# Optimization experiments

Measured on AMD Instinct MI355X. Metric: run time of the kernel, lower is better.

Reference implementation:

```python
import jax, jax.numpy as jnp
import numpy as np

# ---- static config (matches init_kwargs) ----
D = 1152      # hidden_size
I = 4608      # mlp intermediate = 4*D
DEPTH = 2     # transformer blocks
SA_DEPTH = 3  # spatial adapter depth
P_LAT = 2     # latent patch size
OUT_C = 8     # in_channels*2 (learn_sigma)
FREQ = 256    # timestep frequency embedding size
NV = 4        # num_views
B = 2         # true batch (BN = B*NV = 8)
LAT = 32      # latent H=W
COND = 512    # conditioning image H=W

# ---- BitNet b1.58 / HGRN primitives ----

def rmsnorm(x, eps=1e-8):
    return x * jax.lax.rsqrt(jnp.mean(jnp.square(x), axis=-1, keepdims=True) + eps)

def layernorm(x, gamma=None, beta=None, eps=1e-6):
    mu = jnp.mean(x, axis=-1, keepdims=True)
    xc = x - mu
    y = xc * jax.lax.rsqrt(jnp.mean(jnp.square(xc), axis=-1, keepdims=True) + eps)
    if gamma is not None:
        y = y * gamma + beta
    return y

def _act_quant(x):  # per-token int8 absmax quantization
    s = 127.0 / jnp.clip(jnp.max(jnp.abs(x), axis=-1, keepdims=True), 1e-5, None)
    return jnp.clip(jnp.round(x * s), -128.0, 127.0) / s

def _w_quant(w):    # ternary (1.58-bit) weight quantization, global absmean scale
    s = 1.0 / jnp.clip(jnp.mean(jnp.abs(w)), 1e-5, None)
    return jnp.clip(jnp.round(w * s), -1.0, 1.0) / s

def _ste(x, q):     # straight-through estimator
    return x + jax.lax.stop_gradient(q - x)

def bitlinear(x, w, b=None):
    # FusedBitLinear: RMSNorm -> int8 act quant -> ternary weight matmul
    xn = rmsnorm(x)
    y = _ste(xn, _act_quant(xn)) @ _ste(w, _w_quant(w)).T
    return y if b is None else y + b

def conv2d(x, w, b, stride):
    y = jax.lax.conv_general_dilated(x, w, (stride, stride), 'VALID',
                                     dimension_numbers=('NCHW', 'OIHW', 'NCHW'))
    return y + b[None, :, None, None]

def hgrn_attn(x, wi, wf, wg, wo):
    # HGRN gated-linear attention: h_t = f_t*h_{t-1} + silu(i_t)*(1-f_t),
    # output RMSNorm-swish-gated then o-projected. Element-wise recurrence.
    f = jax.nn.sigmoid(bitlinear(x, wf))
    v = jax.nn.silu(bitlinear(x, wi)) * (1.0 - f)
    g = bitlinear(x, wg)
    def step(h, fv):
        ft, vt = fv
        h = ft * h + vt
        return h, h
    _, o = jax.lax.scan(step, jnp.zeros_like(v[:, 0]),
                        (jnp.swapaxes(f, 0, 1), jnp.swapaxes(v, 0, 1)))
    o = jnp.swapaxes(o, 0, 1)
    o = rmsnorm(o) * g * jax.nn.sigmoid(g)
    return bitlinear(o, wo)

def hgrn_mlp(x, w_gate, w_down):
    gate, y = jnp.split(bitlinear(x, w_gate), 2, axis=-1)
    return bitlinear(jax.nn.silu(gate) * y, w_down)

def modulate(x, shift, scale):
    return x * (1.0 + scale[:, None]) + shift[:, None]

# ---- full adapter forward ----

def _forward(x, t, y, x_cond, ref_tokens, num_views, P):
    BN = x.shape[0]
    # conditioning vector c = TimestepEmbedder(t) + prompt_proj(y)
    half = FREQ // 2
    freqs = jnp.exp(-np.log(10000.0) * jnp.arange(half, dtype=jnp.float32) / half)
    ang = t[:, None] * freqs[None]
    t_emb = jnp.concatenate([jnp.cos(ang), jnp.sin(ang)], axis=-1)
    t_emb = bitlinear(jax.nn.silu(bitlinear(t_emb, P['te_w1'], P['te_b1'])), P['te_w2'], P['te_b2'])
    c = t_emb + bitlinear(y, P['pp_w'], P['pp_b'])

    h = conv2d(x_cond, P['sa_pe_w'], P['sa_pe_b'], 16)      # [BN, D, 32, 32]
    Hc = h.shape[-1]
    h = h.reshape(BN, D, Hc * Hc).transpose(0, 2, 1)
    feats = []
    for i in range(SA_DEPTH):
        h = hgrn_mlp(layernorm(h, P['sa_ln_g'][i], P['sa_ln_b'][i], eps=1e-5),
                     P['sa_gate_w'][i], P['sa_down_w'][i])
        h = h.transpose(0, 2, 1).reshape(BN, D, Hc, Hc)
        h = conv2d(h, P['sa_dc_w'][i], P['sa_dc_b'][i], 2)
        Hc //= 2
        h = h.reshape(BN, D, Hc * Hc).transpose(0, 2, 1)
        feats.append(h)

    # patchify latents + pos embed + spatial cond feature (grid-matched)
    xt = conv2d(x, P['xe_w'], P['xe_b'], P_LAT)             # [BN, D, 16, 16]
    Hp = xt.shape[-1]
    xt = xt.reshape(BN, D, Hp * Hp).transpose(0, 2, 1) + P['pos_embed'] + feats[0]
    L = xt.shape[1]
    b = BN // num_views
    ref_rep = jnp.repeat(ref_tokens, num_views, axis=0)     # repeat_interleave dim 0

    for l in range(DEPTH):
        mod = bitlinear(jax.nn.silu(c), P['blk_ada_w'][l], P['blk_ada_b'][l])
        sh_a, sc_a, g_a, sh_m, sc_m, g_m = jnp.split(mod, 6, axis=-1)
        xm = modulate(layernorm(xt), sh_a, sc_a)
        self_out = hgrn_attn(xm, P['blk_sa_wi'][l], P['blk_sa_wf'][l], P['blk_sa_wg'][l], P['blk_sa_wo'][l])
        # multi-view attention: sequence axis = views
        mv_in = xm.reshape(b, num_views, L, D).transpose(0, 2, 1, 3).reshape(b * L, num_views, D)
        mv_out = hgrn_attn(mv_in, P['blk_mv_wi'][l], P['blk_mv_wf'][l], P['blk_mv_wg'][l], P['blk_mv_wo'][l])
        mv_out = mv_out.reshape(b, L, num_views, D).transpose(0, 2, 1, 3).reshape(BN, L, D)
        ref_out = hgrn_attn(ref_rep, P['blk_rf_wi'][l], P['blk_rf_wf'][l], P['blk_rf_wg'][l], P['blk_rf_wo'][l])
        xt = xt + g_a[:, None] * (self_out + mv_out + ref_out)
        xm = modulate(layernorm(xt), sh_m, sc_m)
        xt = xt + g_m[:, None] * hgrn_mlp(xm, P['blk_gate_w'][l], P['blk_down_w'][l])

    # final layer + unpatchify
    mod = bitlinear(jax.nn.silu(c), P['fl_ada_w'], P['fl_ada_b'])
    shift, scale = jnp.split(mod, 2, axis=-1)
    xt = bitlinear(modulate(layernorm(xt), shift, scale), P['fl_w'], P['fl_b'])
    xt = xt.reshape(BN, Hp, Hp, P_LAT, P_LAT, OUT_C).transpose(0, 5, 1, 3, 2, 4)
    return xt.reshape(BN, OUT_C, Hp * P_LAT, Hp * P_LAT)

PARAM_SHAPES = {
    'xe_w': (D, 4, P_LAT, P_LAT), 'xe_b': (D,), 'pos_embed': (1, 256, D),
    'te_w1': (D, FREQ), 'te_b1': (D,), 'te_w2': (D, D), 'te_b2': (D,),
    'pp_w': (D, 768), 'pp_b': (D,),
    'sa_pe_w': (D, 6, 16, 16), 'sa_pe_b': (D,),
    'sa_ln_g': (SA_DEPTH, D), 'sa_ln_b': (SA_DEPTH, D),
    'sa_gate_w': (SA_DEPTH, 2 * I, D), 'sa_down_w': (SA_DEPTH, D, I),
    'sa_dc_w': (SA_DEPTH, D, D, 2, 2), 'sa_dc_b': (SA_DEPTH, D),
    'blk_ada_w': (DEPTH, 6 * D, D), 'blk_ada_b': (DEPTH, 6 * D),
    'blk_sa_wi': (DEPTH, D, D), 'blk_sa_wf': (DEPTH, D, D), 'blk_sa_wg': (DEPTH, D, D), 'blk_sa_wo': (DEPTH, D, D),
    'blk_mv_wi': (DEPTH, D, D), 'blk_mv_wf': (DEPTH, D, D), 'blk_mv_wg': (DEPTH, D, D), 'blk_mv_wo': (DEPTH, D, D),
    'blk_rf_wi': (DEPTH, D, D), 'blk_rf_wf': (DEPTH, D, D), 'blk_rf_wg': (DEPTH, D, D), 'blk_rf_wo': (DEPTH, D, D),
    'blk_gate_w': (DEPTH, 2 * I, D), 'blk_down_w': (DEPTH, D, I),
    'fl_w': (P_LAT * P_LAT * OUT_C, D), 'fl_b': (P_LAT * P_LAT * OUT_C,),
    'fl_ada_w': (2 * D, D), 'fl_ada_b': (2 * D,),
}
_ZEROS = {'xe_b', 'te_b1', 'te_b2', 'pp_b', 'sa_pe_b', 'sa_ln_b', 'sa_dc_b',
          'blk_ada_b', 'fl_b', 'fl_ada_b'}
_ONES = {'sa_ln_g'}

def setup_inputs() -> dict:
    key = jax.random.key(0)
    ks = iter(jax.random.split(key, 8 + len(PARAM_SHAPES)))
    inp = {
        'x': jax.random.normal(next(ks), (B * NV, 4, LAT, LAT), jnp.float32),
        't': jax.random.uniform(next(ks), (B * NV,), jnp.float32, 0.0, 1000.0),
        'y': jax.random.normal(next(ks), (B * NV, 768), jnp.float32),
        'x_cond': jax.random.normal(next(ks), (B * NV, 6, COND, COND), jnp.float32),
        'ref_tokens': jax.random.normal(next(ks), (B, 256, D), jnp.float32),
        'num_views': NV,
    }
    for name, shp in PARAM_SHAPES.items():
        if name in _ZEROS:
            inp[name] = jnp.zeros(shp, jnp.float32)
        elif name in _ONES:
            inp[name] = jnp.ones(shp, jnp.float32)
        else:
            inp[name] = 0.02 * jax.random.normal(next(ks), shp, jnp.float32)
    return inp

def reference(x, t, y, x_cond, ref_tokens, num_views,
              xe_w, xe_b, pos_embed, te_w1, te_b1, te_w2, te_b2, pp_w, pp_b,
              sa_pe_w, sa_pe_b, sa_ln_g, sa_ln_b, sa_gate_w, sa_down_w, sa_dc_w, sa_dc_b,
              blk_ada_w, blk_ada_b,
              blk_sa_wi, blk_sa_wf, blk_sa_wg, blk_sa_wo,
              blk_mv_wi, blk_mv_wf, blk_mv_wg, blk_mv_wo,
              blk_rf_wi, blk_rf_wf, blk_rf_wg, blk_rf_wo,
              blk_gate_w, blk_down_w, fl_w, fl_b, fl_ada_w, fl_ada_b):
    P = dict(xe_w=xe_w, xe_b=xe_b, pos_embed=pos_embed, te_w1=te_w1, te_b1=te_b1,
             te_w2=te_w2, te_b2=te_b2, pp_w=pp_w, pp_b=pp_b, sa_pe_w=sa_pe_w,
             sa_pe_b=sa_pe_b, sa_ln_g=sa_ln_g, sa_ln_b=sa_ln_b, sa_gate_w=sa_gate_w,
             sa_down_w=sa_down_w, sa_dc_w=sa_dc_w, sa_dc_b=sa_dc_b, blk_ada_w=blk_ada_w,
             blk_ada_b=blk_ada_b, blk_sa_wi=blk_sa_wi, blk_sa_wf=blk_sa_wf,
             blk_sa_wg=blk_sa_wg, blk_sa_wo=blk_sa_wo, blk_mv_wi=blk_mv_wi,
             blk_mv_wf=blk_mv_wf, blk_mv_wg=blk_mv_wg, blk_mv_wo=blk_mv_wo,
             blk_rf_wi=blk_rf_wi, blk_rf_wf=blk_rf_wf, blk_rf_wg=blk_rf_wg,
             blk_rf_wo=blk_rf_wo, blk_gate_w=blk_gate_w, blk_down_w=blk_down_w,
             fl_w=fl_w, fl_b=fl_b, fl_ada_w=fl_ada_w, fl_ada_b=fl_ada_b)
    return _forward(x, t, y, x_cond, ref_tokens, int(num_views), P)
```

## Files before the change

### kernel.cpp

```cpp
#include <hip/hip_runtime.h>

#define DEV __device__ __forceinline__

typedef __attribute__((ext_vector_type(4))) int i32x4;
typedef __attribute__((ext_vector_type(4))) double f64x4;


struct WList { const float* p[37]; long long n[37]; };
struct WOffs { long long o[37]; };
struct W3 { const signed char* w[3]; const double* sc[3]; double* c[3]; };

DEV int2 xcd_swz(int gridx)
{
    const int nwg = (int)gridDim.x, b = (int)blockIdx.x;
    const int q = nwg >> 3, r = nwg & 7, xcd = b & 7, idx = b >> 3;
    const int lb = (xcd < r ? xcd*(q+1) : r*(q+1) + (xcd-r)*q) + idx;
    return make_int2(lb % gridx, lb / gridx);
}

__global__ void k_mfma64_probe(double* __restrict__ out)
{
    const int lane = threadIdx.x;
    double a = (double)(1 + lane);
    double b = (double)(101 + 3*lane);
    f64x4 acc = {0.0, 0.0, 0.0, 0.0};
    acc = __builtin_amdgcn_mfma_f64_16x16x4f64(a, b, acc, 0, 0, 0);
#pragma unroll
    for (int r = 0; r < 4; ++r) out[lane*4 + r] = acc[r];
}

__global__ void k_mfma64_check(const double* __restrict__ probe, int* __restrict__ flag)
{
    if (threadIdx.x != 0) return;
// ... 185 lines not shown
    for (int s = 128; s > 0; s >>= 1) { if (tid < s) red[tid] += red[tid+s]; __syncthreads(); }
    double rmso = 1.0 / sqrt(red[0]/(double)K + 1e-8);
    __syncthreads();
    double ss2 = 0.0, am = 0.0;
    for (int i = tid; i < K; i += 256) {
        double g = grow[i];
        double y = rb[i]*rmso * g / (1.0 + exp(-g));
        rb[i] = y; ss2 += y*y; am = fmax(am, fabs(y));
    }
    red[tid] = ss2; red2[tid] = am;
    __syncthreads();
    for (int s = 128; s > 0; s >>= 1) {
        if (tid < s) { red[tid] += red[tid+s]; red2[tid] = fmax(red2[tid], red2[tid+s]); }
        __syncthreads();
    }
    double rms = 1.0 / sqrt(red[0]/(double)K + 1e-8);
    double s   = 127.0 / fmax(red2[0]*rms, 1e-5);
    signed char* qrow = q8 + (size_t)row*K;
    for (int i = tid; i < K; i += 256)
        qrow[i] = (signed char)(int)fmin(fmax(rint(rb[i]*rms*s), -128.0), 127.0);
    if (tid == 0) dscale[row] = s;
}

__global__ void k_gatepre(double* __restrict__ F, double* __restrict__ I, long long n)
{
    long long i = (long long)blockIdx.x*256 + threadIdx.x;
    if (i >= n) return;
    double fp = F[i], ip = I[i];
    double f = 1.0/(1.0+exp(-fp));
    double v = (ip/(1.0+exp(-ip)))*(1.0-f);
    F[i] = f; I[i] = v;
}

__global__ void k_scan2(const double* __restrict__ F, const double* __restrict__ V,
                        double* __restrict__ O, int n_outer, long long outer_stride,
                        int n_inner, long long t_stride, int T)
{
    long long chain = (long long)blockIdx.x*blockDim.x + threadIdx.x;
    if (chain >= (long long)n_outer*n_inner) return;
    long long base = (chain / n_inner)*outer_stride + (chain % n_inner);
    double h = 0.0;
    for (int t = 0; t < T; ++t) {
        long long idx = base + (long long)t*t_stride;
        h = F[idx]*h + V[idx];
        O[idx] = h;
    }
}

__global__ void k_scan3(const double* __restrict__ F, const double* __restrict__ Isilu,
                        double* __restrict__ O, int n_outer, long long outer_stride,
                        int n_inner, long long t_stride, int T)
{
    long long chain = (long long)blockIdx.x*blockDim.x + threadIdx.x;
    if (chain >= (long long)n_outer*n_inner) return;
    long long base = (chain / n_inner)*outer_stride + (chain % n_inner);
    double h = 0.0;
    for (int t = 0; t < T; ++t) {
        long long idx = base + (long long)t*t_stride;
        double f = F[idx];
        double v = Isilu[idx]*(1.0-f);
        h = f*h + v;
        O[idx] = h;
    }
}

__global__ void k_add(const double* __restrict__ a, const double* __restrict__ b,
                      double* __restrict__ o, int n)
{
    int i = blockIdx.x*256 + threadIdx.x;
    if (i < n) o[i] = a[i] + b[i];
}

__global__ void k_resid_attn(double* __restrict__ xt, const double* __restrict__ acc,
                             const double* __restrict__ refo, const double* __restrict__ mod)
{
    int idx = blockIdx.x*256 + threadIdx.x;
    int r = idx / 1152, d = idx - r*1152;
    int bn = r >> 8, l = r & 255;
    double ga = mod[(size_t)bn*6912 + 2*1152 + d];
    double rv = refo[((size_t)((bn>>2)*256 + l))*1152 + d];
    xt[idx] += ga*(acc[idx] + rv);
}

__global__ void k_resid_mlp(double* __restrict__ xt, const double* __restrict__ t2,
                            const double* __restrict__ mod)
{
    int idx = blockIdx.x*256 + threadIdx.x;
    int r = idx / 1152, d = idx - r*1152;
    int bn = r >> 8;
    xt[idx] += mod[(size_t)bn*6912 + 5*1152 + d] * t2[idx];
}

__global__ void k_patchify(const float* __restrict__ x, const float* __restrict__ w,
                           const float* __restrict__ bias, const float* __restrict__ pos,
                           const double* __restrict__ f0, double* __restrict__ xt)
{
    int idx = blockIdx.x*256 + threadIdx.x;
    int r = idx / 1152, o = idx - r*1152;
    int bn = r >> 8, p = r & 255;
    int y = p >> 4, xx = p & 15;
    double acc = (double)bias[o] + (double)pos[(size_t)p*1152 + o] + f0[idx];
#pragma unroll
    for (int c = 0; c < 4; ++c)
#pragma unroll
// ... 34 lines not shown
}

template<int WMODE>
DEV void load_w4d(const float* __restrict__ W, int row, int k, int Nb, int K, double o[4])
{
    if (row >= Nb) { o[0]=o[1]=o[2]=o[3]=0.0; return; }
    if constexpr (WMODE == 0) {
        float4 v = *reinterpret_cast<const float4*>(W + (size_t)row*K + k);
        o[0]=v.x; o[1]=v.y; o[2]=v.z; o[3]=v.w;
    } else {
        int q = k/1152, c = k - q*1152;
        const float* p = W + (size_t)row*4608 + (size_t)c*4 + q;
        o[0]=p[0]; o[1]=p[4]; o[2]=p[8]; o[3]=p[12];
    }
}

template<int AMODE, int WMODE>
__global__ __launch_bounds__(256)
void k_dgemm(const void* __restrict__ A, const float* __restrict__ W,
             const float* __restrict__ bias, double* __restrict__ C,
             int M, int N, int K, int gridx, const int* __restrict__ mfma_flag)
{
    __shared__ double As[64][33];
    __shared__ double Ws[64][33];
    const int tid = threadIdx.x;
    const int2 bxy = xcd_swz(gridx);
    const int m0 = bxy.y*64, n0 = bxy.x*64;
    const int lr = tid >> 2;
    const int lc = (tid & 3) * 4;
    const int flag = *mfma_flag;

    if (flag) {
        const int cmb = flag - 1;
        const int a_alt = cmb & 1, b_alt = (cmb >> 1) & 1, dv = (cmb >> 2) & 3;
        const int lane = tid & 63, wid = tid >> 6;
        const int wm = wid >> 1, wn = wid & 1;
        const int ai = a_alt ? (lane >> 2) : (lane & 15);
        const int ak = a_alt ? (lane & 3)  : (lane >> 4);
        const int bj = b_alt ? (lane >> 2) : (lane & 15);
        const int bk = b_alt ? (lane & 3)  : (lane >> 4);
        f64x4 fa[2][2];
#pragma unroll
        for (int i = 0; i < 2; ++i)
#pragma unroll
            for (int j = 0; j < 2; ++j) fa[i][j] = f64x4{0.0,0.0,0.0,0.0};

        for (int kt = 0; kt < K; kt += 32) {
#pragma unroll
            for (int h = 0; h < 2; ++h) {
                double v[4];
                load_a4d<AMODE>(A, m0+lr, kt + h*16 + lc, M, v);
                As[lr][h*16+lc+0]=v[0]; As[lr][h*16+lc+1]=v[1];
                As[lr][h*16+lc+2]=v[2]; As[lr][h*16+lc+3]=v[3];
                double wv[4];
                load_w4d<WMODE>(W, n0+lr, kt + h*16 + lc, N, K, wv);
                Ws[lr][h*16+lc+0]=wv[0]; Ws[lr][h*16+lc+1]=wv[1];
                Ws[lr][h*16+lc+2]=wv[2]; Ws[lr][h*16+lc+3]=wv[3];
            }
            __syncthreads();
#pragma unroll
            for (int k4 = 0; k4 < 8; ++k4) {
                double a0 = As[wm*32 + ai][k4*4 + ak];
                double a1 = As[wm*32 + 16 + ai][k4*4 + ak];
                double b0 = Ws[wn*32 + bj][k4*4 + bk];
                double b1 = Ws[wn*32 + 16 + bj][k4*4 + bk];
                fa[0][0] = __builtin_amdgcn_mfma_f64_16x16x4f64(a0, b0, fa[0][0], 0, 0, 0);
                fa[0][1] = __builtin_amdgcn_mfma_f64_16x16x4f64(a0, b1, fa[0][1], 0, 0, 0);
                fa[1][0] = __builtin_amdgcn_mfma_f64_16x16x4f64(a1, b0, fa[1][0], 0, 0, 0);
                fa[1][1] = __builtin_amdgcn_mfma_f64_16x16x4f64(a1, b1, fa[1][1], 0, 0, 0);
            }
            __syncthreads();
        }
#pragma unroll
        for (int i = 0; i < 2; ++i)
#pragma unroll
            for (int j = 0; j < 2; ++j)
#pragma unroll
                for (int r = 0; r < 4; ++r) {
                    int ir = (dv & 2) ? (4*r + (lane >> 4)) : (4*(lane >> 4) + r);
                    int ic = lane & 15;
                    if (dv & 1) { int t = ir; ir = ic; ic = t; }
                    int row = m0 + wm*32 + i*16 + ir;
                    int col = n0 + wn*32 + j*16 + ic;
                    if (row < M && col < N)
                        C[(size_t)row*N + col] = fa[i][j][r] + (bias ? (double)bias[col] : 0.0);
                }
        return;
    }

    const int tx = tid & 15, ty = tid >> 4;
    double acc[4][4] = {};
    for (int kt = 0; kt < K; kt += 16) {
        {
            double v[4];
            load_a4d<AMODE>(A, m0+lr, kt+lc, M, v);
            As[lr][lc+0]=v[0]; As[lr][lc+1]=v[1]; As[lr][lc+2]=v[2]; As[lr][lc+3]=v[3];
        }
        {
            double wv[4];
            load_w4d<WMODE>(W, n0+lr, kt+lc, N, K, wv);
            Ws[lr][lc+0]=wv[0]; Ws[lr][lc+1]=wv[1]; Ws[lr][lc+2]=wv[2]; Ws[lr][lc+3]=wv[3];
        }
        __syncthreads();
#pragma unroll
        for (int k = 0; k < 16; ++k) {
            double a[4], b[4];
#pragma unroll
            for (int e = 0; e < 4; ++e) { a[e] = As[ty + 16*e][k]; b[e] = Ws[tx + 16*e][k]; }
#pragma unroll
            for (int i = 0; i < 4; ++i)
#pragma unroll
                for (int j = 0; j < 4; ++j) acc[i][j] += a[i]*b[j];
        }
        __syncthreads();
    }
#pragma unroll
    for (int i = 0; i < 4; ++i) {
        int row = m0 + ty + 16*i;
        if (row >= M) continue;
#pragma unroll
        for (int j = 0; j < 4; ++j) {
            int col = n0 + tx + 16*j;
            if (col >= N) continue;
            C[(size_t)row*N + col] = acc[i][j] + (bias ? (double)bias[col] : 0.0);
        }
    }
}

template<int GATE, int PRE>
__global__ __launch_bounds__(256)
void k_qgemm(const signed char* __restrict__ A8, const double* __restrict__ ascale,
             const float* __restrict__ Wf, const signed char* __restrict__ W8,
             const double* __restrict__ wsum, long long wcount,
             const float* __restrict__ bias, double* __restrict__ C,
             int M, int N, int K, int accum, int gridM)
{
    __shared__ __align__(16) signed char Als[8][128][16];
    __shared__ __align__(16) signed char Bls[8][128][16];
    __shared__ __align__(16) signed char B2ls[GATE?8:1][GATE?128:1][16];
    const int tid = threadIdx.x;
    const int lane = tid & 63, wid = tid >> 6;
    const int wr = wid >> 1, wc = wid & 1;
    const int2 bxy = xcd_swz(gridM);
    const int m0 = bxy.x*128, n0 = bxy.y*128;
    const int ks = lane >> 4, fr = lane & 15;

    const double dqw = fmax(*wsum / (double)wcount, 1e-5);
    const double thr = 0.5 * dqw;
// ... 105 lines not shown
        for (int r = 0; r < 4; ++r) {
            int row = m0 + wr*64 + i*16 + (lane>>4)*4 + r;
            if (row >= M) continue;
            double mul = dqw / ascale[row];
#pragma unroll
            for (int j = 0; j < 4; ++j) {
                int col = n0 + wc*64 + j*16 + (lane & 15);
                if (col >= N) continue;
                size_t o = (size_t)row*N + col;
                if constexpr (GATE) {
                    double g = (double)acc[i][j][r] * mul;
                    double y = (double)acc2[i][j][r] * mul;
                    C[o] = g/(1.0+exp(-g)) * y;
                } else {
                    double v = (double)acc[i][j][r] * mul;
                    if (bias) v += (double)bias[col];
                    C[o] = accum ? C[o] + v : v;
                }
            }
        }
    }
}

__global__ __launch_bounds__(256)
void k_qgemm3(const signed char* __restrict__ A8, const double* __restrict__ ascale,
              W3 w3, long long wcount, int M, int gridM)
{
    __shared__ __align__(16) signed char Als[8][128][16];
    __shared__ __align__(16) signed char Bls[8][128][16];
    const int tid = threadIdx.x;
    const int lane = tid & 63, wid = tid >> 6;
    const int wr = wid >> 1, wc = wid & 1;
    const int2 bxy = xcd_swz(gridM);
    const int m0 = bxy.x*128;
    const int yy = bxy.y;
    const int g = yy / 9, nt = yy - g*9;
    const int n0 = nt*128;
    const signed char* W8 = w3.w[g];
    double* C = w3.c[g];
    const int ks = lane >> 4, fr = lane & 15;

    const double dqw = fmax(*w3.sc[g] / (double)wcount, 1e-5);

    i32x4 acc[4][4];
#pragma unroll
    for (int i = 0; i < 4; ++i)
#pragma unroll
        for (int j = 0; j < 4; ++j) acc[i][j] = i32x4{0,0,0,0};

    for (int kt = 0; kt < 1152; kt += 128) {
#pragma unroll
        for (int c = 0; c < 4; ++c) {
            int idx = tid + c*256;
            int row = idx & 127, kslot = idx >> 7;
            i32x4 v = {0,0,0,0};
            if (m0 + row < M)
                v = *reinterpret_cast<const i32x4*>(A8 + (size_t)(m0+row)*1152 + kt + kslot*16);
            *reinterpret_cast<i32x4*>(&Als[kslot][row][0]) = v;
        }
#pragma unroll
        for (int c = 0; c < 4; ++c) {
            int idx = tid + c*256;
            int row = idx & 127, kslot = idx >> 7;
            i32x4 pv = *reinterpret_cast<const i32x4*>(W8 + (size_t)(n0+row)*1152 + kt + kslot*16);
            *reinterpret_cast<i32x4*>(&Bls[kslot][row][0]) = pv;
        }
        __syncthreads();
#pragma unroll
        for (int kk = 0; kk < 2; ++kk) {
            const int kb = kk*4 + ks;
            i32x4 a[4];
#pragma unroll
            for (int i = 0; i < 4; ++i)
                a[i] = *reinterpret_cast<const i32x4*>(&Als[kb][wr*64 + i*16 + fr][0]);
#pragma unroll
            for (int j = 0; j < 4; ++j) {
                i32x4 b = *reinterpret_cast<const i32x4*>(&Bls[kb][wc*64 + j*16 + fr][0]);
#pragma unroll
                for (int i = 0; i < 4; ++i)
                    acc[i][j] = __builtin_amdgcn_mfma_i32_16x16x64_i8(a[i], b, acc[i][j], 0, 0, 0);
            }
        }
        __syncthreads();
    }

#pragma unroll
    for (int i = 0; i < 4; ++i) {
#pragma unroll
        for (int r = 0; r < 4; ++r) {
            int row = m0 + wr*64 + i*16 + (lane>>4)*4 + r;
            if (row >= M) continue;
            double mul = dqw / ascale[row];
#pragma unroll
            for (int j = 0; j < 4; ++j) {
                int col = n0 + wc*64 + j*16 + (lane & 15);
                double v = (double)acc[i][j][r] * mul;
                if (g == 0)      v = 1.0/(1.0+exp(-v));
                else if (g == 1) v = v/(1.0+exp(-v));
                C[(size_t)row*1152 + col] = v;
            }
        }
    }
}

extern "C" void kernel_launch(void* const* d_in, const int* in_sizes, int n_in,
                              void* d_out, int out_size, void* d_ws, size_t ws_size,
                              hipStream_t stream)
{
    (void)in_sizes; (void)n_in; (void)out_size;
    auto in = [&](int i){ return (const float*)d_in[i]; };

    const float *X = in(0), *T = in(1), *Y = in(2), *XC = in(3), *REF = in(4);
    const float *xe_w = in(6), *xe_b = in(7), *pos = in(8);
    const float *te_w1 = in(9), *te_b1 = in(10), *te_w2 = in(11), *te_b2 = in(12);
    const float *pp_w = in(13), *pp_b = in(14);
    const float *sa_pe_w = in(15), *sa_pe_b = in(16);
    const float *sa_ln_g = in(17), *sa_ln_b = in(18);
    const float *sa_gate_w = in(19), *sa_down_w = in(20);
    const float *sa_dc_w = in(21), *sa_dc_b = in(22);
    const float *ada_w = in(23), *ada_b = in(24);
    const float *sa_wi = in(25), *sa_wf = in(26), *sa_wg = in(27), *sa_wo = in(28);
    const float *mv_wi = in(29), *mv_wf = in(30), *mv_wg = in(31), *mv_wo = in(32);
    const float *rf_wi = in(33), *rf_wf = in(34), *rf_wg = in(35), *rf_wo = in(36);
    const float *gate_w = in(37), *down_w = in(38);
    const float *fl_w = in(39), *fl_b = in(40), *fl_ada_w = in(41), *fl_ada_b = in(42);
    float* OUT = (float*)d_out;

    size_t off = 0;
    auto AL = [&](size_t bytes){ off = (off+255)&~(size_t)255; size_t r = off; off += bytes; return r; };
    const size_t oScale = AL(37*8);
    const size_t oPart  = AL(37*32*8);
    const size_t oProbe = AL(64*4*8);
    const size_t oFlag  = AL(256);
    const size_t oSM1 = AL(8*1152*8), oSM2 = AL(8*1152*8), oSM3 = AL(8*1152*8);
    const size_t oCB  = AL(8*1152*8);
    const size_t oMOD = AL(8*6912*8);
    const size_t oH   = AL((size_t)8192*1152*8);
    const size_t oINT = AL((size_t)1024*4608*8);
    const size_t oF0  = AL((size_t)2048*1152*8);
    const size_t oXT  = AL((size_t)2048*1152*8);
    const size_t oFB  = AL((size_t)2048*1152*8);
    const size_t oIB  = AL((size_t)2048*1152*8);
    const size_t oGB  = AL((size_t)2048*1152*8);
    const size_t oRO  = AL((size_t)512*1152*8);
    const size_t oQ8X = AL((size_t)2048*1152);
    const size_t oQ8I = AL((size_t)1024*4608);
    const size_t oQ8O = AL((size_t)2048*1152);
    const size_t oQ8R = AL((size_t)512*1152);
    const size_t oQ8T = AL((size_t)8*1152);
    const size_t oQ8C = AL((size_t)8*1152);
    const size_t oDSX = AL(2048*8), oDSI = AL(1024*8), oDSO = AL(2048*8);
    const size_t oDSR = AL(512*8),  oDST = AL(8*8),    oDSC = AL(8*8);
    if (off > ws_size) return;

    WList wl{}; WOffs wo{};
    long long wn[37];
    int nw = 0;
    auto addw = [&](const float* w, long long n){ wl.p[nw]=w; wl.n[nw]=n; wn[nw]=n; nw++; };
    addw(te_w1, 294912); addw(te_w2, 1327104); addw(pp_w, 884736);
    addw(sa_gate_w, 10616832); addw(sa_down_w, 5308416);
    for (int l = 0; l < 2; ++l) {
        addw(ada_w + (size_t)l*7962624, 7962624);
        addw(sa_wi + (size_t)l*1327104, 1327104);
        addw(sa_wf + (size_t)l*1327104, 1327104);
        addw(sa_wg + (size_t)l*1327104, 1327104);
        addw(sa_wo + (size_t)l*1327104, 1327104);
        addw(mv_wi + (size_t)l*1327104, 1327104);
        addw(mv_wf + (size_t)l*1327104, 1327104);
        addw(mv_wg + (size_t)l*1327104, 1327104);
        addw(mv_wo + (size_t)l*1327104, 1327104);
        addw(rf_wi + (size_t)l*1327104, 1327104);
        addw(rf_wf + (size_t)l*1327104, 1327104);
        addw(rf_wg + (size_t)l*1327104, 1327104);
        addw(rf_wo + (size_t)l*1327104, 1327104);
// ... 19 lines not shown
    if (useW8) {
        size_t off_w8 = off;
        oINTb = AL((size_t)4096*4608*8); oQ8Ib = AL((size_t)4096*4608);
        oQ8Xb = AL((size_t)4096*1152);   oDSXb = AL(4096*8); oDSIb = AL(4096*8);
        if (off <= ws_size) schunk = 4096;
        else {
            off = off_w8;
            oINTb = AL((size_t)2048*4608*8); oQ8Ib = AL((size_t)2048*4608); oDSIb = AL(2048*8);
            if (off <= ws_size) schunk = 2048;
            else off = off_w8;
        }
    }

    char* w8p = (char*)d_ws;
    double* scales = (double*)(w8p + oScale);
    double* parts  = (double*)(w8p + oPart);
    double* probeD = (double*)(w8p + oProbe);
    int*    mflag  = (int*)(w8p + oFlag);
    double *SM1=(double*)(w8p+oSM1), *SM2=(double*)(w8p+oSM2), *SM3=(double*)(w8p+oSM3);
    double *CB=(double*)(w8p+oCB), *MOD=(double*)(w8p+oMOD);
    double *H=(double*)(w8p+oH), *INT=(double*)(w8p+oINT);
    double *F0=(double*)(w8p+oF0), *XT=(double*)(w8p+oXT);
    double *FB=(double*)(w8p+oFB), *IB=(double*)(w8p+oIB), *GB=(double*)(w8p+oGB);
    double *ACC=F0, *OB=H, *RO=(double*)(w8p+oRO);
    signed char *Q8X=(signed char*)(w8p+oQ8X), *Q8I=(signed char*)(w8p+oQ8I);
    signed char *Q8O=(signed char*)(w8p+oQ8O), *Q8R=(signed char*)(w8p+oQ8R);
    signed char *Q8T=(signed char*)(w8p+oQ8T), *Q8C=(signed char*)(w8p+oQ8C);
    double *DSX=(double*)(w8p+oDSX), *DSI=(double*)(w8p+oDSI), *DSO=(double*)(w8p+oDSO);
    double *DSR=(double*)(w8p+oDSR), *DST=(double*)(w8p+oDST), *DSC=(double*)(w8p+oDSC);
    signed char* W8 = (signed char*)(w8p + oW8);
    float* Wt = (float*)(w8p + oWt);

    double*      INTs = (schunk > 1024) ? (double*)(w8p + oINTb) : INT;
    signed char* Q8Is = (schunk > 1024) ? (signed char*)(w8p + oQ8Ib) : Q8I;
    double*      DSIs = (schunk > 1024) ? (double*)(w8p + oDSIb) : DSI;
    signed char* Q8Xs = (schunk == 4096) ? (signed char*)(w8p + oQ8Xb) : Q8X;
    double*      DSXs = (schunk == 4096) ? (double*)(w8p + oDSXb) : DSX;

    k_mfma64_probe<<<1, 64, 0, stream>>>(probeD);
    k_mfma64_check<<<1, 64, 0, stream>>>(probeD, mflag);
    k_abssum_all<<<dim3(32,37), 256, 0, stream>>>(wl, parts);
    k_abssum_fin<<<37, 64, 0, stream>>>(parts, scales);
    if (useW8)
        k_ternarize<<<dim3(64,37), 256, 0, stream>>>(wl, wo, scales, W8);
    if (useWt)
        k_dcw_prep<<<1152, 256, 0, stream>>>(sa_dc_w, Wt);

    auto qgemm = [&](const signed char* A8, const double* as, const float* Win, int slot,
                     const float* b, double* Cout, int M, int N, int K, int accum){
        int gm = (M+127)/128, gn = (N+127)/128;
        if (useW8)
// ... 25 lines not shown
            long long nch = (long long)n_outer*n_inner;
            k_scan3<<<(unsigned)((nch+255)/256), 256, 0, stream>>>(FB, IB, OB, n_outer, ostr, n_inner, tstr, Tlen);
        } else {
            qgemm(A8, as, wF, sF, nullptr, FB, M, 1152, 1152, 0);
            qgemm(A8, as, wI, sI, nullptr, IB, M, 1152, 1152, 0);
            qgemm(A8, as, wG, sG, nullptr, GB, M, 1152, 1152, 0);
            long long nel = (long long)M*1152;
            k_gatepre<<<(unsigned)((nel+255)/256), 256, 0, stream>>>(FB, IB, nel);
            long long nch = (long long)n_outer*n_inner;
            k_scan2<<<(unsigned)((nch+255)/256), 256, 0, stream>>>(FB, IB, OB, n_outer, ostr, n_inner, tstr, Tlen);
        }
    };

    k_temb<<<8, 128, 0, stream>>>(T, SM1);
    k_rsq8<double><<<8, 256, 0, stream>>>(SM1, Q8T, DST, 256, 0);
    qgemm(Q8T, DST, te_w1, 0, te_b1, SM3, 8, 1152, 256, 0);
    k_rsq8<double><<<8, 256, 0, stream>>>(SM3, Q8T, DST, 1152, 1);
    qgemm(Q8T, DST, te_w2, 1, te_b2, SM2, 8, 1152, 1152, 0);
    k_rsq8<float><<<8, 256, 0, stream>>>(Y, Q8T, DST, 768, 0);
    qgemm(Q8T, DST, pp_w, 2, pp_b, SM3, 8, 1152, 768, 0);
    k_add<<<36, 256, 0, stream>>>(SM2, SM3, CB, 9216);
    k_rsq8<double><<<8, 256, 0, stream>>>(CB, Q8C, DSC, 1152, 1);

    k_dgemm<1,0><<<18*128, 256, 0, stream>>>(XC, sa_pe_w, sa_pe_b, H, 8192, 1152, 1536, 18, mflag);
    {
        const int nch = 8192 / schunk;
        for (int ch = 0; ch < nch; ++ch) {
            double* Hrow = H + (size_t)ch*schunk*1152;
            k_lnq8<<<schunk, 256, 1152*8, stream>>>(Hrow, Q8Xs, DSXs, 1152, sa_ln_g, sa_ln_b,
                                                    nullptr, nullptr, 0, 1e-5);
            qgemmGate(Q8Xs, DSXs, sa_gate_w, 3, INTs, schunk);
            k_rsq8<double><<<schunk, 256, 0, stream>>>(INTs, Q8Is, DSIs, 4608, 0);
            qgemm(Q8Is, DSIs, sa_down_w, 4, nullptr, Hrow, schunk, 1152, 4608, 0);
        }
    }
    if (useWt)
        k_dgemm<2,0><<<18*32, 256, 0, stream>>>(H, Wt, sa_dc_b, F0, 2048, 1152, 4608, 18, mflag);
    else
        k_dgemm<2,1><<<18*32, 256, 0, stream>>>(H, sa_dc_w, sa_dc_b, F0, 2048, 1152, 4608, 18, mflag);

    k_patchify<<<9216, 256, 0, stream>>>(X, xe_w, xe_b, pos, F0, XT);
    k_rsq8<float><<<512, 256, 0, stream>>>(REF, Q8R, DSR, 1152, 0);

    for (int l = 0; l < 2; ++l) {
        int sb = 5 + l*15;
        const float *wada = ada_w + (size_t)l*7962624, *bada = ada_b + (size_t)l*6912;
        const float *swi = sa_wi + (size_t)l*1327104, *swf = sa_wf + (size_t)l*1327104;
        const float *swg = sa_wg + (size_t)l*1327104, *swo = sa_wo + (size_t)l*1327104;
        const float *mwi = mv_wi + (size_t)l*1327104, *mwf = mv_wf + (size_t)l*1327104;
        const float *mwg = mv_wg + (size_t)l*1327104, *mwo = mv_wo + (size_t)l*1327104;
        const float *rwi = rf_wi + (size_t)l*1327104, *rwf = rf_wf + (size_t)l*1327104;
        const float *rwg = rf_wg + (size_t)l*1327104, *rwo = rf_wo + (size_t)l*1327104;
        const float *wgt = gate_w + (size_t)l*10616832, *wdn = down_w + (size_t)l*5308416;

        qgemm(Q8C, DSC, wada, sb+0, bada, MOD, 8, 6912, 1152, 0);

        k_lnq8<<<2048, 256, 1152*8, stream>>>(XT, Q8X, DSX, 1152, nullptr, nullptr,
                                              MOD+0, MOD+1152, 6912, 1e-6);

        fig(Q8X, DSX, sb+2, sb+1, sb+3, swf, swi, swg, 2048, 8, 294912LL, 1152, 1152LL, 256);
        k_ogateq8<<<2048, 256, 1152*8, stream>>>(OB, GB, Q8O, DSO, 1152);
        qgemm(Q8O, DSO, swo, sb+4, nullptr, ACC, 2048, 1152, 1152, 0);

        fig(Q8X, DSX, sb+6, sb+5, sb+7, mwf, mwi, mwg, 2048, 2, 1179648LL, 294912, 294912LL, 4);
        k_ogateq8<<<2048, 256, 1152*8, stream>>>(OB, GB, Q8O, DSO, 1152);
        qgemm(Q8O, DSO, mwo, sb+8, nullptr, ACC, 2048, 1152, 1152, 1);

        fig(Q8R, DSR, sb+10, sb+9, sb+11, rwf, rwi, rwg, 512, 2, 294912LL, 1152, 1152LL, 256);
        k_ogateq8<<<512, 256, 1152*8, stream>>>(OB, GB, Q8O, DSO, 1152);
        qgemm(Q8O, DSO, rwo, sb+12, nullptr, RO, 512, 1152, 1152, 0);

        k_resid_attn<<<9216, 256, 0, stream>>>(XT, ACC, RO, MOD);

        k_lnq8<<<2048, 256, 1152*8, stream>>>(XT, Q8X, DSX, 1152, nullptr, nullptr,
                                              MOD+3*1152, MOD+4*1152, 6912, 1e-6);
        if (schunk >= 2048) {
            qgemmGate(Q8X, DSX, wgt, sb+13, INTs, 2048);
            k_rsq8<double><<<2048, 256, 0, stream>>>(INTs, Q8Is, DSIs, 4608, 0);
            qgemm(Q8Is, DSIs, wdn, sb+14, nullptr, OB, 2048, 1152, 4608, 0);
        } else {
            for (int ch = 0; ch < 2; ++ch) {
                qgemmGate(Q8X + (size_t)ch*1024*1152, DSX + ch*1024, wgt, sb+13, INT, 1024);
                k_rsq8<double><<<1024, 256, 0, stream>>>(INT, Q8I, DSI, 4608, 0);
                qgemm(Q8I, DSI, wdn, sb+14, nullptr, OB + (size_t)ch*1024*1152, 1024, 1152, 4608, 0);
            }
        }
        k_resid_mlp<<<9216, 256, 0, stream>>>(XT, OB, MOD);
    }

    qgemm(Q8C, DSC, fl_ada_w, 35, fl_ada_b, MOD, 8, 2304, 1152, 0);
    k_lnq8<<<2048, 256, 1152*8, stream>>>(XT, Q8X, DSX, 1152, nullptr, nullptr,
                                          MOD+0, MOD+1152, 2304, 1e-6);
    qgemm(Q8X, DSX, fl_w, 36, fl_b, FB, 2048, 32, 1152, 0);
    k_unpatch<<<256, 256, 0, stream>>>(FB, OUT);
}
// ... 1 lines not shown
```

Measured before the change: 4.703 ms.

## Batch spatial and multiview HGRN branches into shared kernels; widen fp64 GEMM N-tile

The spatial-attention and multi-view HGRN branches take the same quantized input, so their six gate projections now run in one grouped int8 GEMM launch. Their two scans, two output-gating quantizations and two output projections are likewise each merged into a single launch, and a new residual kernel adds both branch outputs. This cuts launch count and fills the GPU better on moderately sized GEMMs. Separately, the fp64 dgemm tile grows from 64 to 128 columns, giving more MFMA work per A load. The cost is extra workspace buffers and more register pressure in the dgemm.

```diff
diff --git a/kernel.cpp b/kernel.cpp
--- a/kernel.cpp
+++ b/kernel.cpp
@@ -9,6 +9,7 @@
 struct WList { const float* p[37]; long long n[37]; };
 struct WOffs { long long o[37]; };
 struct W3 { const signed char* w[3]; const double* sc[3]; double* c[3]; };
+struct W6 { const signed char* w[6]; const double* sc[6]; double* c[6]; };
 
 DEV int2 xcd_swz(int gridx)
 {
@@ -240,6 +241,42 @@
     if (tid == 0) dscale[row] = s;
 }
 
+__global__ void k_ogateq8c(const double* __restrict__ Os, const double* __restrict__ Gs,
+                           const double* __restrict__ Om, const double* __restrict__ Gm,
+                           signed char* __restrict__ q8, double* __restrict__ dscale)
+{
+    extern __shared__ double rb[];
+    __shared__ double red[256], red2[256];
+    const int row = blockIdx.x, tid = threadIdx.x;
+    const int K = 1152;
+    const double* orow = (row < 2048) ? (Os + (size_t)row*K) : (Om + (size_t)(row-2048)*K);
+    const double* grow = (row < 2048) ? (Gs + (size_t)row*K) : (Gm + (size_t)(row-2048)*K);
+    double ss = 0.0;
+    for (int i = tid; i < K; i += 256) { double v = orow[i]; rb[i] = v; ss += v*v; }
+    red[tid] = ss; __syncthreads();
+    for (int s = 128; s > 0; s >>= 1) { if (tid < s) red[tid] += red[tid+s]; __syncthreads(); }
+    double rmso = 1.0 / sqrt(red[0]/(double)K + 1e-8);
+    __syncthreads();
+    double ss2 = 0.0, am = 0.0;
+    for (int i = tid; i < K; i += 256) {
+        double g = grow[i];
+        double y = rb[i]*rmso * g / (1.0 + exp(-g));
+        rb[i] = y; ss2 += y*y; am = fmax(am, fabs(y));
+    }
+    red[tid] = ss2; red2[tid] = am;
+    __syncthreads();
+    for (int s = 128; s > 0; s >>= 1) {
+        if (tid < s) { red[tid] += red[tid+s]; red2[tid] = fmax(red2[tid], red2[tid+s]); }
+        __syncthreads();
+    }
+    double rms = 1.0 / sqrt(red[0]/(double)K + 1e-8);
+    double s   = 127.0 / fmax(red2[0]*rms, 1e-5);
+    signed char* qrow = q8 + (size_t)row*K;
+    for (int i = tid; i < K; i += 256)
+        qrow[i] = (signed char)(int)fmin(fmax(rint(rb[i]*rms*s), -128.0), 127.0);
+    if (tid == 0) dscale[row] = s;
+}
+
 __global__ void k_gatepre(double* __restrict__ F, double* __restrict__ I, long long n)
 {
     long long i = (long long)blockIdx.x*256 + threadIdx.x;
@@ -282,6 +319,36 @@
     }
 }
 
+__global__ void k_scanc(const double* __restrict__ Fs, const double* __restrict__ Is,
+                        const double* __restrict__ Fm, const double* __restrict__ Im,
+                        double* __restrict__ Osf, double* __restrict__ Omv)
+{
+    long long cid = (long long)blockIdx.x*blockDim.x + threadIdx.x;
+    if (cid < 9216) {
+        long long base = (cid / 1152)*294912LL + (cid % 1152);
+        double h = 0.0;
+        for (int t = 0; t < 256; ++t) {
+            long long idx = base + (long long)t*1152;
+            double f = Fs[idx];
+            double v = Is[idx]*(1.0-f);
+            h = f*h + v;
+            Osf[idx] = h;
+        }
+    } else {
+        long long c2 = cid - 9216;
+        if (c2 >= 589824LL) return;
+        long long base = (c2 / 294912)*1179648LL + (c2 % 294912);
+        double h = 0.0;
+        for (int t = 0; t < 4; ++t) {
+            long long idx = base + (long long)t*294912;
+            double f = Fm[idx];
+            double v = Im[idx]*(1.0-f);
+            h = f*h + v;
+            Omv[idx] = h;
+        }
+    }
+}
+
 __global__ void k_add(const double* __restrict__ a, const double* __restrict__ b,
                       double* __restrict__ o, int n)
 {
@@ -298,6 +365,18 @@
     double ga = mod[(size_t)bn*6912 + 2*1152 + d];
     double rv = refo[((size_t)((bn>>2)*256 + l))*1152 + d];
     xt[idx] += ga*(acc[idx] + rv);
+}
+
+__global__ void k_resid_attn2(double* __restrict__ xt, const double* __restrict__ acc,
+                              const double* __restrict__ mvb, const double* __restrict__ refo,
+                              const double* __restrict__ mod)
+{
+    int idx = blockIdx.x*256 + threadIdx.x;
+    int r = idx / 1152, d = idx - r*1152;
+    int bn = r >> 8, l = r & 255;
+    double ga = mod[(size_t)bn*6912 + 2*1152 + d];
+    double rv = refo[((size_t)((bn>>2)*256 + l))*1152 + d];
+    xt[idx] += ga*((acc[idx] + mvb[idx]) + rv);
 }
 
 __global__ void k_resid_mlp(double* __restrict__ xt, const double* __restrict__ t2,
@@ -378,12 +457,14 @@
              int M, int N, int K, int gridx, const int* __restrict__ mfma_flag)
 {
     __shared__ double As[64][33];
-    __shared__ double Ws[64][33];
+    __shared__ double Ws[128][33];
     const int tid = threadIdx.x;
     const int2 bxy = xcd_swz(gridx);
-    const int m0 = bxy.y*64, n0 = bxy.x*64;
+    const int m0 = bxy.y*64, n0 = bxy.x*128;
     const int lr = tid >> 2;
     const int lc = (tid & 3) * 4;
+    const int wrow = tid >> 1;
+    const int wkb = (tid & 1) * 16;
     const int flag = *mfma_flag;
 
     if (flag) {
@@ -395,11 +476,11 @@
         const int ak = a_alt ? (lane & 3)  : (lane >> 4);
         const int bj = b_alt ? (lane >> 2) : (lane & 15);
         const int bk = b_alt ? (lane & 3)  : (lane >> 4);
-        f64x4 fa[2][2];
+        f64x4 fa[2][4];
 #pragma unroll
         for (int i = 0; i < 2; ++i)
 #pragma unroll
-            for (int j = 0; j < 2; ++j) fa[i][j] = f64x4{0.0,0.0,0.0,0.0};
+            for (int j = 0; j < 4; ++j) fa[i][j] = f64x4{0.0,0.0,0.0,0.0};
 
         for (int kt = 0; kt < K; kt += 32) {
 #pragma unroll
@@ -408,36 +489,41 @@
                 load_a4d<AMODE>(A, m0+lr, kt + h*16 + lc, M, v);
                 As[lr][h*16+lc+0]=v[0]; As[lr][h*16+lc+1]=v[1];
                 As[lr][h*16+lc+2]=v[2]; As[lr][h*16+lc+3]=v[3];
+            }
+#pragma unroll
+            for (int qd = 0; qd < 4; ++qd) {
                 double wv[4];
-                load_w4d<WMODE>(W, n0+lr, kt + h*16 + lc, N, K, wv);
-                Ws[lr][h*16+lc+0]=wv[0]; Ws[lr][h*16+lc+1]=wv[1];
-                Ws[lr][h*16+lc+2]=wv[2]; Ws[lr][h*16+lc+3]=wv[3];
+                load_w4d<WMODE>(W, n0+wrow, kt + wkb + qd*4, N, K, wv);
+                Ws[wrow][wkb+qd*4+0]=wv[0]; Ws[wrow][wkb+qd*4+1]=wv[1];
+                Ws[wrow][wkb+qd*4+2]=wv[2]; Ws[wrow][wkb+qd*4+3]=wv[3];
             }
             __syncthreads();
 #pragma unroll
             for (int k4 = 0; k4 < 8; ++k4) {
                 double a0 = As[wm*32 + ai][k4*4 + ak];
                 double a1 = As[wm*32 + 16 + ai][k4*4 + ak];
-                double b0 = Ws[wn*32 + bj][k4*4 + bk];
-                double b1 = Ws[wn*32 + 16 + bj][k4*4 + bk];
-                fa[0][0] = __builtin_amdgcn_mfma_f64_16x16x4f64(a0, b0, fa[0][0], 0, 0, 0);
-                fa[0][1] = __builtin_amdgcn_mfma_f64_16x16x4f64(a0, b1, fa[0][1], 0, 0, 0);
-                fa[1][0] = __builtin_amdgcn_mfma_f64_16x16x4f64(a1, b0, fa[1][0], 0, 0, 0);
-                fa[1][1] = __builtin_amdgcn_mfma_f64_16x16x4f64(a1, b1, fa[1][1], 0, 0, 0);
+                double b[4];
+#pragma unroll
+                for (int j = 0; j < 4; ++j) b[j] = Ws[wn*64 + j*16 + bj][k4*4 + bk];
+#pragma unroll
+                for (int j = 0; j < 4; ++j) {
+                    fa[0][j] = __builtin_amdgcn_mfma_f64_16x16x4f64(a0, b[j], fa[0][j], 0, 0, 0);
+                    fa[1][j] = __builtin_amdgcn_mfma_f64_16x16x4f64(a1, b[j], fa[1][j], 0, 0, 0);
+                }
             }
             __syncthreads();
         }
 #pragma unroll
         for (int i = 0; i < 2; ++i)
 #pragma unroll
-            for (int j = 0; j < 2; ++j)
+            for (int j = 0; j < 4; ++j)
 #pragma unroll
                 for (int r = 0; r < 4; ++r) {
                     int ir = (dv & 2) ? (4*r + (lane >> 4)) : (4*(lane >> 4) + r);
                     int ic = lane & 15;
                     if (dv & 1) { int t = ir; ir = ic; ic = t; }
                     int row = m0 + wm*32 + i*16 + ir;
-                    int col = n0 + wn*32 + j*16 + ic;
+                    int col = n0 + wn*64 + j*16 + ic;
                     if (row < M && col < N)
                         C[(size_t)row*N + col] = fa[i][j][r] + (bias ? (double)bias[col] : 0.0);
                 }
@@ -445,41 +531,44 @@
     }
 
     const int tx = tid & 15, ty = tid >> 4;
-    double acc[4][4] = {};
-    for (int kt = 0; kt < K; kt += 16) {
-        {
-            double v[4];
-            load_a4d<AMODE>(A, m0+lr, kt+lc, M, v);
-            As[lr][lc+0]=v[0]; As[lr][lc+1]=v[1]; As[lr][lc+2]=v[2]; As[lr][lc+3]=v[3];
-        }
-        {
-            double wv[4];
-            load_w4d<WMODE>(W, n0+lr, kt+lc, N, K, wv);
-            Ws[lr][lc+0]=wv[0]; Ws[lr][lc+1]=wv[1]; Ws[lr][lc+2]=wv[2]; Ws[lr][lc+3]=wv[3];
+    for (int nh = 0; nh < 2; ++nh) {
+        double acc[4][4] = {};
+        for (int kt = 0; kt < K; kt += 16) {
+            {
+                double v[4];
+                load_a4d<AMODE>(A, m0+lr, kt+lc, M, v);
+                As[lr][lc+0]=v[0]; As[lr][lc+1]=v[1]; As[lr][lc+2]=v[2]; As[lr][lc+3]=v[3];
+            }
+            {
+                double wv[4];
+                load_w4d<WMODE>(W, n0 + nh*64 + lr, kt+lc, N, K, wv);
+                Ws[lr][lc+0]=wv[0]; Ws[lr][lc+1]=wv[1]; Ws[lr][lc+2]=wv[2]; Ws[lr][lc+3]=wv[3];
+            }
+            __syncthreads();
+#pragma unroll
+            for (int k = 0; k < 16; ++k) {
+                double a[4], b[4];
+#pragma unroll
+                for (int e = 0; e < 4; ++e) { a[e] = As[ty + 16*e][k]; b[e] = Ws[tx + 16*e][k]; }
+#pragma unroll
+                for (int i = 0; i < 4; ++i)
+#pragma unroll
+                    for (int j = 0; j < 4; ++j) acc[i][j] += a[i]*b[j];
+            }
+            __syncthreads();
+        }
+#pragma unroll
+        for (int i = 0; i < 4; ++i) {
+            int row = m0 + ty + 16*i;
+            if (row >= M) continue;
+#pragma unroll
+            for (int j = 0; j < 4; ++j) {
+                int col = n0 + nh*64 + tx + 16*j;
+                if (col >= N) continue;
+                C[(size_t)row*N + col] = acc[i][j] + (bias ? (double)bias[col] : 0.0);
+            }
         }
         __syncthreads();
-#pragma unroll
-        for (int k = 0; k < 16; ++k) {
-            double a[4], b[4];
-#pragma unroll
-            for (int e = 0; e < 4; ++e) { a[e] = As[ty + 16*e][k]; b[e] = Ws[tx + 16*e][k]; }
-#pragma unroll
-            for (int i = 0; i < 4; ++i)
-#pragma unroll
-                for (int j = 0; j < 4; ++j) acc[i][j] += a[i]*b[j];
-        }
-        __syncthreads();
-    }
-#pragma unroll
-    for (int i = 0; i < 4; ++i) {
-        int row = m0 + ty + 16*i;
-        if (row >= M) continue;
-#pragma unroll
-        for (int j = 0; j < 4; ++j) {
-            int col = n0 + tx + 16*j;
-            if (col >= N) continue;
-            C[(size_t)row*N + col] = acc[i][j] + (bias ? (double)bias[col] : 0.0);
-        }
     }
 }
 
@@ -631,9 +720,10 @@
     }
 }
 
-__global__ __launch_bounds__(256)
-void k_qgemm3(const signed char* __restrict__ A8, const double* __restrict__ ascale,
-              W3 w3, long long wcount, int M, int gridM)
+template<int NG>
+DEV void qgemmN_body(const signed char* __restrict__ A8, const double* __restrict__ ascale,
+                     const signed char* const* w, const double* const* sc,
+                     double* const* cc, long long wcount, int M, int gridM)
 {
     __shared__ __align__(16) signed char Als[8][128][16];
     __shared__ __align__(16) signed char Bls[8][128][16];
@@ -645,11 +735,11 @@
     const int yy = bxy.y;
     const int g = yy / 9, nt = yy - g*9;
     const int n0 = nt*128;
-    const signed char* W8 = w3.w[g];
-    double* C = w3.c[g];
+    const signed char* W8 = w[g];
+    double* C = cc[g];
     const int ks = lane >> 4, fr = lane & 15;
 
-    const double dqw = fmax(*w3.sc[g] / (double)wcount, 1e-5);
+    const double dqw = fmax(*sc[g] / (double)wcount, 1e-5);
 
     i32x4 acc[4][4];
 #pragma unroll
@@ -693,6 +783,7 @@
         __syncthreads();
     }
 
+    const int gm3 = g % 3;
 #pragma unroll
     for (int i = 0; i < 4; ++i) {
 #pragma unroll
@@ -704,9 +795,103 @@
             for (int j = 0; j < 4; ++j) {
                 int col = n0 + wc*64 + j*16 + (lane & 15);
                 double v = (double)acc[i][j][r] * mul;
-                if (g == 0)      v = 1.0/(1.0+exp(-v));
-                else if (g == 1) v = v/(1.0+exp(-v));
+                if (gm3 == 0)      v = 1.0/(1.0+exp(-v));
+                else if (gm3 == 1) v = v/(1.0+exp(-v));
                 C[(size_t)row*1152 + col] = v;
+            }
+        }
+    }
+}
+
+__global__ __launch_bounds__(256)
+void k_qgemm3(const signed char* __restrict__ A8, const double* __restrict__ ascale,
+              W3 w3, long long wcount, int M, int gridM)
+{
+    qgemmN_body<3>(A8, ascale, w3.w, w3.sc, w3.c, wcount, M, gridM);
+}
+
+__global__ __launch_bounds__(256)
+void k_qgemm6(const signed char* __restrict__ A8, const double* __restrict__ ascale,
+              W6 w6, long long wcount, int M, int gridM)
+{
+    qgemmN_body<6>(A8, ascale, w6.w, w6.sc, w6.c, wcount, M, gridM);
+}
+
+__global__ __launch_bounds__(256)
+void k_qgemmO(const signed char* __restrict__ A8, const double* __restrict__ ascale,
+              const signed char* __restrict__ Ws8, const signed char* __restrict__ Wm8,
+              const double* __restrict__ scs, const double* __restrict__ scm,
+              long long wcount, double* __restrict__ Cs, double* __restrict__ Cm,
+              int gridM)
+{
+    __shared__ __align__(16) signed char Als[8][128][16];
+    __shared__ __align__(16) signed char Bls[8][128][16];
+    const int tid = threadIdx.x;
+    const int lane = tid & 63, wid = tid >> 6;
+    const int wr = wid >> 1, wc = wid & 1;
+    const int2 bxy = xcd_swz(gridM);
+    const int m0 = bxy.x*128;
+    const int yy = bxy.y;
+    const int sel = (yy < 9) ? 0 : 1;
+    const int n0 = (sel ? (yy-9) : yy)*128;
+    const signed char* W8 = sel ? Wm8 : Ws8;
+    const signed char* A  = A8 + (sel ? (size_t)2048*1152 : 0);
+    const double* as = ascale + (sel ? 2048 : 0);
+    double* C = sel ? Cm : Cs;
+    const int ks = lane >> 4, fr = lane & 15;
+
+    const double dqw = fmax((sel ? *scm : *scs) / (double)wcount, 1e-5);
+
+    i32x4 acc[4][4];
+#pragma unroll
+    for (int i = 0; i < 4; ++i)
+#pragma unroll
+        for (int j = 0; j < 4; ++j) acc[i][j] = i32x4{0,0,0,0};
+
+    for (int kt = 0; kt < 1152; kt += 128) {
+#pragma unroll
+        for (int c = 0; c < 4; ++c) {
+            int idx = tid + c*256;
+            int row = idx & 127, kslot = idx >> 7;
+            i32x4 v = *reinterpret_cast<const i32x4*>(A + (size_t)(m0+row)*1152 + kt + kslot*16);
+            *reinterpret_cast<i32x4*>(&Als[kslot][row][0]) = v;
+        }
+#pragma unroll
+        for (int c = 0; c < 4; ++c) {
+            int idx = tid + c*256;
+            int row = idx & 127, kslot = idx >> 7;
+            i32x4 pv = *reinterpret_cast<const i32x4*>(W8 + (size_t)(n0+row)*1152 + kt + kslot*16);
+            *reinterpret_cast<i32x4*>(&Bls[kslot][row][0]) = pv;
+        }
+        __syncthreads();
+#pragma unroll
+        for (int kk = 0; kk < 2; ++kk) {
+            const int kb = kk*4 + ks;
+            i32x4 a[4];
+#pragma unroll
+            for (int i = 0; i < 4; ++i)
+                a[i] = *reinterpret_cast<const i32x4*>(&Als[kb][wr*64 + i*16 + fr][0]);
+#pragma unroll
+            for (int j = 0; j < 4; ++j) {
+                i32x4 b = *reinterpret_cast<const i32x4*>(&Bls[kb][wc*64 + j*16 + fr][0]);
+#pragma unroll
+                for (int i = 0; i < 4; ++i)
+                    acc[i][j] = __builtin_amdgcn_mfma_i32_16x16x64_i8(a[i], b, acc[i][j], 0, 0, 0);
+            }
+        }
+        __syncthreads();
+    }
+
+#pragma unroll
+    for (int i = 0; i < 4; ++i) {
+#pragma unroll
+        for (int r = 0; r < 4; ++r) {
+            int row = m0 + wr*64 + i*16 + (lane>>4)*4 + r;
+            double mul = dqw / as[row];
+#pragma unroll
+            for (int j = 0; j < 4; ++j) {
+                int col = n0 + wc*64 + j*16 + (lane & 15);
+                C[(size_t)row*1152 + col] = (double)acc[i][j][r] * mul;
             }
         }
     }
@@ -751,14 +936,17 @@
     const size_t oFB  = AL((size_t)2048*1152*8);
     const size_t oIB  = AL((size_t)2048*1152*8);
     const size_t oGB  = AL((size_t)2048*1152*8);
+    const size_t oGB2 = AL((size_t)2048*1152*8);
     const size_t oRO  = AL((size_t)512*1152*8);
     const size_t oQ8X = AL((size_t)2048*1152);
     const size_t oQ8I = AL((size_t)1024*4608);
     const size_t oQ8O = AL((size_t)2048*1152);
+    const size_t oQ8O2= AL((size_t)4096*1152);
     const size_t oQ8R = AL((size_t)512*1152);
     const size_t oQ8T = AL((size_t)8*1152);
     const size_t oQ8C = AL((size_t)8*1152);
     const size_t oDSX = AL(2048*8), oDSI = AL(1024*8), oDSO = AL(2048*8);
+    const size_t oDSO2= AL(4096*8);
     const size_t oDSR = AL(512*8),  oDST = AL(8*8),    oDSC = AL(8*8);
     if (off > ws_size) return;
 
@@ -824,11 +1012,17 @@
     double *H=(double*)(w8p+oH), *INT=(double*)(w8p+oINT);
     double *F0=(double*)(w8p+oF0), *XT=(double*)(w8p+oXT);
     double *FB=(double*)(w8p+oFB), *IB=(double*)(w8p+oIB), *GB=(double*)(w8p+oGB);
+    double *GB2=(double*)(w8p+oGB2);
     double *ACC=F0, *OB=H, *RO=(double*)(w8p+oRO);
+    double *FB2 = INT, *IB2 = INT + (size_t)2048*1152;
+    double *MVB = FB2;
+    double *OBs = OB, *OBm = OB + (size_t)2048*1152;
     signed char *Q8X=(signed char*)(w8p+oQ8X), *Q8I=(signed char*)(w8p+oQ8I);
-    signed char *Q8O=(signed char*)(w8p+oQ8O), *Q8R=(signed char*)(w8p+oQ8R);
+    signed char *Q8O=(signed char*)(w8p+oQ8O), *Q8O2=(signed char*)(w8p+oQ8O2);
+    signed char *Q8R=(signed char*)(w8p+oQ8R);
     signed char *Q8T=(signed char*)(w8p+oQ8T), *Q8C=(signed char*)(w8p+oQ8C);
     double *DSX=(double*)(w8p+oDSX), *DSI=(double*)(w8p+oDSI), *DSO=(double*)(w8p+oDSO);
+    double *DSO2=(double*)(w8p+oDSO2);
     double *DSR=(double*)(w8p+oDSR), *DST=(double*)(w8p+oDST), *DSC=(double*)(w8p+oDSC);
     signed char* W8 = (signed char*)(w8p + oW8);
     float* Wt = (float*)(w8p + oWt);
@@ -900,7 +1094,7 @@
     k_add<<<36, 256, 0, stream>>>(SM2, SM3, CB, 9216);
     k_rsq8<double><<<8, 256, 0, stream>>>(CB, Q8C, DSC, 1152, 1);
 
-    k_dgemm<1,0><<<18*128, 256, 0, stream>>>(XC, sa_pe_w, sa_pe_b, H, 8192, 1152, 1536, 18, mflag);
+    k_dgemm<1,0><<<9*128, 256, 0, stream>>>(XC, sa_pe_w, sa_pe_b, H, 8192, 1152, 1536, 9, mflag);
     {
         const int nch = 8192 / schunk;
         for (int ch = 0; ch < nch; ++ch) {
@@ -913,9 +1107,9 @@
         }
     }
     if (useWt)
-        k_dgemm<2,0><<<18*32, 256, 0, stream>>>(H, Wt, sa_dc_b, F0, 2048, 1152, 4608, 18, mflag);
+        k_dgemm<2,0><<<9*32, 256, 0, stream>>>(H, Wt, sa_dc_b, F0, 2048, 1152, 4608, 9, mflag);
     else
-        k_dgemm<2,1><<<18*32, 256, 0, stream>>>(H, sa_dc_w, sa_dc_b, F0, 2048, 1152, 4608, 18, mflag);
+        k_dgemm<2,1><<<9*32, 256, 0, stream>>>(H, sa_dc_w, sa_dc_b, F0, 2048, 1152, 4608, 9, mflag);
 
     k_patchify<<<9216, 256, 0, stream>>>(X, xe_w, xe_b, pos, F0, XT);
     k_rsq8<float><<<512, 256, 0, stream>>>(REF, Q8R, DSR, 1152, 0);
@@ -936,19 +1130,33 @@
         k_lnq8<<<2048, 256, 1152*8, stream>>>(XT, Q8X, DSX, 1152, nullptr, nullptr,
                                               MOD+0, MOD+1152, 6912, 1e-6);
 
-        fig(Q8X, DSX, sb+2, sb+1, sb+3, swf, swi, swg, 2048, 8, 294912LL, 1152, 1152LL, 256);
-        k_ogateq8<<<2048, 256, 1152*8, stream>>>(OB, GB, Q8O, DSO, 1152);
-        qgemm(Q8O, DSO, swo, sb+4, nullptr, ACC, 2048, 1152, 1152, 0);
-
-        fig(Q8X, DSX, sb+6, sb+5, sb+7, mwf, mwi, mwg, 2048, 2, 1179648LL, 294912, 294912LL, 4);
-        k_ogateq8<<<2048, 256, 1152*8, stream>>>(OB, GB, Q8O, DSO, 1152);
-        qgemm(Q8O, DSO, mwo, sb+8, nullptr, ACC, 2048, 1152, 1152, 1);
-
-        fig(Q8R, DSR, sb+10, sb+9, sb+11, rwf, rwi, rwg, 512, 2, 294912LL, 1152, 1152LL, 256);
-        k_ogateq8<<<512, 256, 1152*8, stream>>>(OB, GB, Q8O, DSO, 1152);
-        qgemm(Q8O, DSO, rwo, sb+12, nullptr, RO, 512, 1152, 1152, 0);
-
-        k_resid_attn<<<9216, 256, 0, stream>>>(XT, ACC, RO, MOD);
+        if (useW8) {
+            W6 w6{ {W8+wo.o[sb+2], W8+wo.o[sb+1], W8+wo.o[sb+3],
+                    W8+wo.o[sb+6], W8+wo.o[sb+5], W8+wo.o[sb+7]},
+                   {scales+sb+2, scales+sb+1, scales+sb+3,
+                    scales+sb+6, scales+sb+5, scales+sb+7},
+                   {FB, IB, GB, FB2, IB2, GB2} };
+            k_qgemm6<<<16*54, 256, 0, stream>>>(Q8X, DSX, w6, 1327104, 2048, 16);
+            k_scanc<<<(9216 + 589824 + 255)/256, 256, 0, stream>>>(FB, IB, FB2, IB2, OBs, OBm);
+            k_ogateq8c<<<4096, 256, 1152*8, stream>>>(OBs, GB, OBm, GB2, Q8O2, DSO2);
+            k_qgemmO<<<16*18, 256, 0, stream>>>(Q8O2, DSO2, W8+wo.o[sb+4], W8+wo.o[sb+8],
+                                                scales+sb+4, scales+sb+8, 1327104, ACC, MVB, 16);
+            fig(Q8R, DSR, sb+10, sb+9, sb+11, rwf, rwi, rwg, 512, 2, 294912LL, 1152, 1152LL, 256);
+            k_ogateq8<<<512, 256, 1152*8, stream>>>(OB, GB, Q8O, DSO, 1152);
+            qgemm(Q8O, DSO, rwo, sb+12, nullptr, RO, 512, 1152, 1152, 0);
+            k_resid_attn2<<<9216, 256, 0, stream>>>(XT, ACC, MVB, RO, MOD);
+        } else {
+            fig(Q8X, DSX, sb+2, sb+1, sb+3, swf, swi, swg, 2048, 8, 294912LL, 1152, 1152LL, 256);
+            k_ogateq8<<<2048, 256, 1152*8, stream>>>(OB, GB, Q8O, DSO, 1152);
+            qgemm(Q8O, DSO, swo, sb+4, nullptr, ACC, 2048, 1152, 1152, 0);
+            fig(Q8X, DSX, sb+6, sb+5, sb+7, mwf, mwi, mwg, 2048, 2, 1179648LL, 294912, 294912LL, 4);
+            k_ogateq8<<<2048, 256, 1152*8, stream>>>(OB, GB, Q8O, DSO, 1152);
+            qgemm(Q8O, DSO, mwo, sb+8, nullptr, ACC, 2048, 1152, 1152, 1);
+            fig(Q8R, DSR, sb+10, sb+9, sb+11, rwf, rwi, rwg, 512, 2, 294912LL, 1152, 1152LL, 256);
+            k_ogateq8<<<512, 256, 1152*8, stream>>>(OB, GB, Q8O, DSO, 1152);
+            qgemm(Q8O, DSO, rwo, sb+12, nullptr, RO, 512, 1152, 1152, 0);
+            k_resid_attn<<<9216, 256, 0, stream>>>(XT, ACC, RO, MOD);
+        }
 
         k_lnq8<<<2048, 256, 1152*8, stream>>>(XT, Q8X, DSX, 1152, nullptr, nullptr,
                                               MOD+3*1152, MOD+4*1152, 6912, 1e-6);
```

New measurement: 4.859 ms. 3.3% more time.
